# Optimization experiments

Measured on AMD Instinct MI355X. Metric: run time of the kernel, lower is better.

## Reference

```python
import jax, jax.numpy as jnp
import numpy as np

NUM_TASKS = 8
NUM_EXPERTS = 8
TOPK = 2
WEX = 0.01
N_TOKENS = 4194304


def setup_inputs() -> dict:
    key = jax.random.key(0)
    k1, k2 = jax.random.split(key)
    router_logits = jax.random.normal(k1, (N_TOKENS, NUM_EXPERTS), dtype=jnp.float32)
    router_labels = jax.random.randint(k2, (N_TOKENS,), 0, NUM_TASKS, dtype=jnp.int64)
    return {"router_logits": router_logits, "router_labels": router_labels}


def reference(router_logits, router_labels):
    # call_update: detached softmax over experts
    probs = jax.lax.stop_gradient(
        jax.nn.softmax(router_logits.astype(jnp.float32), axis=-1)
    )  # [N, E]
    labels = router_labels.astype(jnp.int32)
    # Torch loop `for task in router_labels` adds segment_sum[task] once per
    # occurrence of task -> EX_task_gate[t] = count[t] * segment_sum[t]
    seg_sum = jax.ops.segment_sum(probs, labels, num_segments=NUM_TASKS)  # [T, E]
    counts = jax.ops.segment_sum(
        jnp.ones((probs.shape[0],), dtype=jnp.float32), labels, num_segments=NUM_TASKS
    )  # [T]
    EX_gate = seg_sum * counts[:, None]  # [T, E]
    # calculate_mutual_information_loss
    tot = EX_gate.sum() / TOPK
    EX_gate = EX_gate / (tot + 0.0001)
    P_TI = EX_gate.sum(axis=1, keepdims=True) + 0.0001  # [T, 1]
    P_EI = EX_gate.sum(axis=0, keepdims=True) + 0.0001  # [1, E]
    expert_loss = -(EX_gate * jnp.log(EX_gate / P_TI / P_EI + 0.0001)).sum()
    return jnp.float32(WEX) * expert_loss
```

## Files before the change

kernel.cpp:

```cpp
#include <hip/hip_runtime.h>
#include <hip/hip_bf16.h>

#define N_TOKENS    4194304
#define NUM_EXPERTS 8
#define NUM_TASKS   8
#define GRID        2048
#define BLOCK       256
#define TOK_PER_THREAD (N_TOKENS / (GRID * BLOCK))

__global__ __launch_bounds__(BLOCK) void mi_reduce_kernel(
    const float* __restrict__ logits,
    const int*   __restrict__ labels,
    float*       __restrict__ ws) {

  float acc[NUM_TASKS][NUM_EXPERTS];
#pragma unroll
  for (int t = 0; t < NUM_TASKS; ++t)
#pragma unroll
    for (int e = 0; e < NUM_EXPERTS; ++e) acc[t][e] = 0.0f;

  const int tid = blockIdx.x * BLOCK + threadIdx.x;
  const int S   = GRID * BLOCK;

#pragma unroll 4
  for (int k = 0; k < TOK_PER_THREAD; ++k) {
    const int i = tid + k * S;
    const float4* rp = reinterpret_cast<const float4*>(logits + (size_t)i * NUM_EXPERTS);
    float4 v0 = rp[0];
    float4 v1 = rp[1];
    int lab = labels[i];

    float l[8] = {v0.x, v0.y, v0.z, v0.w, v1.x, v1.y, v1.z, v1.w};
    float mx = fmaxf(fmaxf(fmaxf(l[0], l[1]), fmaxf(l[2], l[3])),
                     fmaxf(fmaxf(l[4], l[5]), fmaxf(l[6], l[7])));
    float p[8];
    float Ssum = 0.0f;
#pragma unroll
    for (int e = 0; e < NUM_EXPERTS; ++e) {
      p[e] = __expf(l[e] - mx);
      Ssum += p[e];
    }
    float r = __builtin_amdgcn_rcpf(Ssum);
#pragma unroll
    for (int e = 0; e < NUM_EXPERTS; ++e) p[e] *= r;

#pragma unroll
    for (int t = 0; t < NUM_TASKS; ++t) {
      float m = (lab == t) ? 1.0f : 0.0f;
#pragma unroll
      for (int e = 0; e < NUM_EXPERTS; ++e)
        acc[t][e] = fmaf(m, p[e], acc[t][e]);
    }
  }

#pragma unroll
  for (int t = 0; t < NUM_TASKS; ++t)
#pragma unroll
    for (int e = 0; e < NUM_EXPERTS; ++e) {
      float v = acc[t][e];
#pragma unroll
      for (int m = 1; m < 64; m <<= 1) v += __shfl_xor(v, m, 64);
      acc[t][e] = v;
    }

  __shared__ float sacc[64];
  if (threadIdx.x < 64) sacc[threadIdx.x] = 0.0f;
  __syncthreads();
  if ((threadIdx.x & 63) == 0) {
#pragma unroll
    for (int t = 0; t < NUM_TASKS; ++t)
#pragma unroll
      for (int e = 0; e < NUM_EXPERTS; ++e)
        atomicAdd(&sacc[t * NUM_EXPERTS + e], acc[t][e]);
  }
  __syncthreads();
  if (threadIdx.x < 64) atomicAdd(&ws[threadIdx.x], sacc[threadIdx.x]);
}

__global__ void mi_finalize_kernel(const float* __restrict__ ws,
                                   float* __restrict__ out) {
  int lane = threadIdx.x;

  float seg = ws[lane];

  float c = seg;
  c += __shfl_xor(c, 1, 64);
  c += __shfl_xor(c, 2, 64);
  c += __shfl_xor(c, 4, 64);

  float ex = seg * c;

  float s = ex;
#pragma unroll
  for (int m = 1; m < 64; m <<= 1) s += __shfl_xor(s, m, 64);
  float tot = s * 0.5f;
  ex = ex / (tot + 1e-4f);

  float pti = ex;
  pti += __shfl_xor(pti, 1, 64);
  pti += __shfl_xor(pti, 2, 64);
  pti += __shfl_xor(pti, 4, 64);
  pti += 1e-4f;

  float pei = ex;
  pei += __shfl_xor(pei, 8, 64);
  pei += __shfl_xor(pei, 16, 64);
  pei += __shfl_xor(pei, 32, 64);
  pei += 1e-4f;

  float term = -ex * logf(ex / pti / pei + 1e-4f);
#pragma unroll
  for (int m = 1; m < 64; m <<= 1) term += __shfl_xor(term, m, 64);

  if (lane == 0) out[0] = 0.01f * term;
}

extern "C" void kernel_launch(void* const* d_in, const int* in_sizes, int n_in,
                              void* d_out, int out_size, void* d_ws, size_t ws_size,
                              hipStream_t stream) {
  const float* logits = (const float*)d_in[0];
  const int*   labels = (const int*)d_in[1];
  float* out = (float*)d_out;
  float* ws  = (float*)d_ws;

  hipMemsetAsync(ws, 0, 64 * sizeof(float), stream);

  mi_reduce_kernel<<<GRID, BLOCK, 0, stream>>>(logits, labels, ws);
  mi_finalize_kernel<<<1, 64, 0, stream>>>(ws, out);
}
```

Before: 232.2 us.

## Split each token across two lanes with coalesced float4 loads and batched loads

Each token's 8 logits are now split across two adjacent lanes. Each lane reads one float4, so consecutive lanes read contiguous memory and loads are fully coalesced. Softmax max and sum are combined with a lane-pair shuffle. The per-thread accumulator shrinks from 64 to 32 registers, which lowers register pressure and the cost of the final warp reduction, and loads are batched four at a time to keep more memory requests in flight. In exchange, each token costs two extra shuffles and each lane does half the work per load.

Result: no change. 232.8 us (+0.2%).

```diff
diff --git a/kernel.cpp b/kernel.cpp
--- a/kernel.cpp
+++ b/kernel.cpp
@@ -6,72 +6,79 @@
 #define NUM_TASKS   8
 #define GRID        2048
 #define BLOCK       256
-#define TOK_PER_THREAD (N_TOKENS / (GRID * BLOCK))
+#define NTHREADS    (GRID * BLOCK)
+#define ITERS       (N_TOKENS * 2 / NTHREADS)
+#define BATCH       4
 
 __global__ __launch_bounds__(BLOCK) void mi_reduce_kernel(
     const float* __restrict__ logits,
     const int*   __restrict__ labels,
     float*       __restrict__ ws) {
 
-  float acc[NUM_TASKS][NUM_EXPERTS];
+  float acc[NUM_TASKS][4];
 #pragma unroll
   for (int t = 0; t < NUM_TASKS; ++t)
 #pragma unroll
-    for (int e = 0; e < NUM_EXPERTS; ++e) acc[t][e] = 0.0f;
+    for (int e = 0; e < 4; ++e) acc[t][e] = 0.0f;
 
-  const int tid = blockIdx.x * BLOCK + threadIdx.x;
-  const int S   = GRID * BLOCK;
-
-#pragma unroll 4
-  for (int k = 0; k < TOK_PER_THREAD; ++k) {
-    const int i = tid + k * S;
-    const float4* rp = reinterpret_cast<const float4*>(logits + (size_t)i * NUM_EXPERTS);
-    float4 v0 = rp[0];
-    float4 v1 = rp[1];
-    int lab = labels[i];
-
-    float l[8] = {v0.x, v0.y, v0.z, v0.w, v1.x, v1.y, v1.z, v1.w};
-    float mx = fmaxf(fmaxf(fmaxf(l[0], l[1]), fmaxf(l[2], l[3])),
-                     fmaxf(fmaxf(l[4], l[5]), fmaxf(l[6], l[7])));
-    float p[8];
-    float Ssum = 0.0f;
-#pragma unroll
-    for (int e = 0; e < NUM_EXPERTS; ++e) {
-      p[e] = __expf(l[e] - mx);
-      Ssum += p[e];
-    }
-    float r = __builtin_amdgcn_rcpf(Ssum);
-#pragma unroll
-    for (int e = 0; e < NUM_EXPERTS; ++e) p[e] *= r;
+  const int u    = blockIdx.x * BLOCK + threadIdx.x;
+  const int tok0 = u >> 1;
+  const float4* __restrict__ lp = reinterpret_cast<const float4*>(logits);
 
 #pragma unroll
-    for (int t = 0; t < NUM_TASKS; ++t) {
-      float m = (lab == t) ? 1.0f : 0.0f;
+  for (int kb = 0; kb < ITERS / BATCH; ++kb) {
+    float4 v[BATCH];
+    int   lab[BATCH];
 #pragma unroll
-      for (int e = 0; e < NUM_EXPERTS; ++e)
-        acc[t][e] = fmaf(m, p[e], acc[t][e]);
+    for (int j = 0; j < BATCH; ++j) {
+      const int k = kb * BATCH + j;
+      v[j]   = lp[(size_t)k * NTHREADS + u];
+      lab[j] = labels[k * (NTHREADS / 2) + tok0];
+    }
+#pragma unroll
+    for (int j = 0; j < BATCH; ++j) {
+      float mx = fmaxf(fmaxf(v[j].x, v[j].y), fmaxf(v[j].z, v[j].w));
+      mx = fmaxf(mx, __shfl_xor(mx, 1, 64));
+      float p0 = __expf(v[j].x - mx);
+      float p1 = __expf(v[j].y - mx);
+      float p2 = __expf(v[j].z - mx);
+      float p3 = __expf(v[j].w - mx);
+      float s = (p0 + p1) + (p2 + p3);
+      s += __shfl_xor(s, 1, 64);
+      float r = __builtin_amdgcn_rcpf(s);
+      p0 *= r; p1 *= r; p2 *= r; p3 *= r;
+#pragma unroll
+      for (int t = 0; t < NUM_TASKS; ++t) {
+        float m = (lab[j] == t) ? 1.0f : 0.0f;
+        acc[t][0] = fmaf(m, p0, acc[t][0]);
+        acc[t][1] = fmaf(m, p1, acc[t][1]);
+        acc[t][2] = fmaf(m, p2, acc[t][2]);
+        acc[t][3] = fmaf(m, p3, acc[t][3]);
+      }
     }
   }
 
 #pragma unroll
   for (int t = 0; t < NUM_TASKS; ++t)
 #pragma unroll
-    for (int e = 0; e < NUM_EXPERTS; ++e) {
-      float v = acc[t][e];
+    for (int e = 0; e < 4; ++e) {
+      float x = acc[t][e];
 #pragma unroll
-      for (int m = 1; m < 64; m <<= 1) v += __shfl_xor(v, m, 64);
-      acc[t][e] = v;
+      for (int m = 2; m < 64; m <<= 1) x += __shfl_xor(x, m, 64);
+      acc[t][e] = x;
     }
 
   __shared__ float sacc[64];
   if (threadIdx.x < 64) sacc[threadIdx.x] = 0.0f;
   __syncthreads();
-  if ((threadIdx.x & 63) == 0) {
+  const int lane = threadIdx.x & 63;
+  if (lane < 2) {
+    const int eoff = lane * 4;
 #pragma unroll
     for (int t = 0; t < NUM_TASKS; ++t)
 #pragma unroll
-      for (int e = 0; e < NUM_EXPERTS; ++e)
-        atomicAdd(&sacc[t * NUM_EXPERTS + e], acc[t][e]);
+      for (int e = 0; e < 4; ++e)
+        atomicAdd(&sacc[t * NUM_EXPERTS + eoff + e], acc[t][e]);
   }
   __syncthreads();
   if (threadIdx.x < 64) atomicAdd(&ws[threadIdx.x], sacc[threadIdx.x]);
```
